# Kernel optimization log

Measured on AMD Instinct MI355X. Metric: run time of the kernel, lower is better.

## Reference

```python
import jax, jax.numpy as jnp
import numpy as np


def gatv2(x, src, dst, ea, Wl, bl, Wr, br, We, att, bias, N):
    # PyG GATv2Conv: source/target projections, edge embedding, leaky_relu(0.2)
    # attention, segment softmax over incoming edges, scatter-add aggregation.
    H, C = att.shape
    xl = (x @ Wl.T + bl).reshape(-1, H, C)   # [N,H,C] (source / message features)
    xr = (x @ Wr.T + br).reshape(-1, H, C)   # [N,H,C] (target features)
    ee = (ea @ We.T).reshape(-1, H, C)       # [E,H,C] edge embedding
    e = jax.nn.leaky_relu(xl[src] + xr[dst] + ee, 0.2)   # [E,H,C]
    s = jnp.einsum('ehc,hc->eh', e, att)                  # [E,H] scores
    smax = jax.ops.segment_max(s, dst, num_segments=N)
    ex = jnp.exp(s - smax[dst])
    den = jax.ops.segment_sum(ex, dst, num_segments=N)
    a = ex / (den[dst] + 1e-16)                           # segment softmax
    out = jax.ops.segment_sum(a[:, :, None] * xl[src], dst, num_segments=N)
    return out.reshape(N, H * C) + bias


def _forward(x, edge_index, edge_attr, actions, Wl1, bl1, Wr1, br1, We1, att1, bias1,
             Wl2, bl2, Wr2, br2, We2, att2, bias2, Wf, bf, Wp, bp, alpha):
    N = x.shape[0]
    E = edge_attr.shape[0]
    num_actions = E + 1
    src, dst = edge_index[0], edge_index[1]
    # add_self_loops(fill_value='mean'): self-loop edge_attr = per-node mean of incoming edge_attr
    cnt = jax.ops.segment_sum(jnp.ones((E,), x.dtype), dst, num_segments=N)
    mean_ea = jax.ops.segment_sum(edge_attr, dst, num_segments=N) / jnp.maximum(cnt, 1.0)[:, None]
    loop = jnp.arange(N, dtype=src.dtype)
    src2 = jnp.concatenate([src, loop])
    dst2 = jnp.concatenate([dst, loop])
    ea2 = jnp.concatenate([edge_attr, mean_ea], axis=0)
    h = jax.nn.relu(gatv2(x, src2, dst2, ea2, Wl1, bl1, Wr1, br1, We1, att1, bias1, N))
    h = jax.nn.relu(gatv2(h, src2, dst2, ea2, Wl2, bl2, Wr2, br2, We2, att2, bias2, N))
    g = jnp.mean(h, axis=0, keepdims=True)              # global_mean_pool, single graph -> [1,hid]
    state_potential = jax.nn.relu(g @ Wp.T + bp)[:, 0]  # [1]
    diag = jnp.concatenate([src != dst, jnp.array([True])])  # [E+1]
    logits = (g @ Wf.T + bf)[:, :num_actions]           # [1, E+1]
    amask = jnp.ones((num_actions,), bool).at[actions].set(False)
    mask = amask & diag
    logits = jnp.where(mask[None, :], logits, -jnp.inf)
    return jax.nn.softmax(logits, axis=1), state_potential, jax.nn.sigmoid(alpha)


def setup_inputs() -> dict:
    key = jax.random.key(0)
    ks = jax.random.split(key, 16)
    N, E, F, hid, H, A = 20000, 400000, 128, 64, 4, 450000
    x = jax.random.normal(ks[0], (N, F), jnp.float32)
    src = jax.random.randint(ks[1], (E,), 0, N)
    dst = (src + 1 + jax.random.randint(ks[2], (E,), 0, N - 1)) % N  # no pre-existing self loops
    edge_index = jnp.stack([src, dst])
    edge_attr = jax.random.normal(ks[3], (E, 1), jnp.float32)
    actions = jax.random.randint(ks[4], (128,), 0, E + 1)
    s = 0.05
    nrm = lambda k, shp: jax.random.normal(k, shp, jnp.float32) * s
    return {
        'x': x, 'edge_index': edge_index, 'edge_attr': edge_attr, 'actions': actions,
        'Wl1': nrm(ks[5], (H * hid, F)), 'bl1': jnp.zeros(H * hid),
        'Wr1': nrm(ks[6], (H * hid, F)), 'br1': jnp.zeros(H * hid),
        'We1': nrm(ks[7], (H * hid, 1)), 'att1': nrm(ks[8], (H, hid)), 'bias1': jnp.zeros(H * hid),
        'Wl2': nrm(ks[9], (hid, H * hid)), 'bl2': jnp.zeros(hid),
        'Wr2': nrm(ks[10], (hid, H * hid)), 'br2': jnp.zeros(hid),
        'We2': nrm(ks[11], (hid, 1)), 'att2': nrm(ks[12], (1, hid)), 'bias2': jnp.zeros(hid),
        'Wf': nrm(ks[13], (A, hid)), 'bf': jnp.zeros(A),
        'Wp': nrm(ks[14], (1, hid)), 'bp': jnp.zeros(1),
        'alpha': jnp.asarray(0.0, jnp.float32),
    }


def reference(x, edge_index, edge_attr, actions, Wl1, bl1, Wr1, br1, We1, att1, bias1,
              Wl2, bl2, Wr2, br2, We2, att2, bias2, Wf, bf, Wp, bp, alpha):
    return _forward(x, edge_index, edge_attr, actions, Wl1, bl1, Wr1, br1, We1, att1, bias1,
                    Wl2, bl2, Wr2, br2, We2, att2, bias2, Wf, bf, Wp, bp, alpha)
```

## Files before the change

### kernel.cpp

```cpp
#include <hip/hip_runtime.h>
#include <math.h>

typedef __attribute__((ext_vector_type(8))) short short8;
typedef __attribute__((ext_vector_type(4))) float f32x4;

__device__ __forceinline__ float wred_sum(float v) {
#pragma unroll
  for (int off = 32; off; off >>= 1) v += __shfl_xor(v, off, 64);
  return v;
}
__device__ __forceinline__ float wred_max(float v) {
#pragma unroll
  for (int off = 32; off; off >>= 1) v = fmaxf(v, __shfl_xor(v, off, 64));
  return v;
}
__device__ __forceinline__ unsigned f2key(float x) {
  unsigned b = __float_as_uint(x);
  return (b & 0x80000000u) ? ~b : (b | 0x80000000u);
}
__device__ __forceinline__ float key2f(unsigned k) {
  unsigned b = (k & 0x80000000u) ? (k & 0x7FFFFFFFu) : ~k;
  return __uint_as_float(b);
}
__device__ __forceinline__ float b2f(unsigned short u) {
  return __uint_as_float(((unsigned)u) << 16);
}
__device__ __forceinline__ unsigned short f2b(float f) {
  unsigned b = __float_as_uint(f);
  return (unsigned short)((b + 0x7FFFu + ((b >> 16) & 1u)) >> 16);
}

__global__ __launch_bounds__(256) void k_prep(
    const float* __restrict__ s0, ushort* __restrict__ d0, int n0,
    const float* __restrict__ s1, ushort* __restrict__ d1, int n1,
    const float* __restrict__ s2, ushort* __restrict__ d2, int n2,
    const float* __restrict__ s3, ushort* __restrict__ d3, int n3,
    const float* __restrict__ s4, ushort* __restrict__ d4, int n4,
    const float* __restrict__ Wf, ushort* __restrict__ wfT8, int NAp,
    const int* __restrict__ dstv, const float* __restrict__ ea,
    int* __restrict__ cnt_i, float* __restrict__ sum_ea, int E,
    int castB, int twfB) {
  __shared__ ushort lds[64][68];
  int b = blockIdx.x, tid = threadIdx.x;
  if (b < castB) {
    int t = (b * 256 + tid) * 4;
    const float* s; ushort* d; int off = t;
    if (off < n0) { s = s0; d = d0; }
    else { off -= n0;
      if (off < n1) { s = s1; d = d1; }
      else { off -= n1;
        if (off < n2) { s = s2; d = d2; }
        else { off -= n2;
          if (off < n3) { s = s3; d = d3; }
          else { off -= n3;
            if (off < n4) { s = s4; d = d4; }
            else return; } } } }
    float4 v = *(const float4*)(s + off);
    ushort4 o;
    o.x = f2b(v.x); o.y = f2b(v.y); o.z = f2b(v.z); o.w = f2b(v.w);
    *(ushort4*)(d + off) = o;
    return;
  }
  if (b < castB + twfB) {
    int row0 = (b - castB) * 64;
    int r = tid >> 2, cg = tid & 3;
    const float* srcp = Wf + ((size_t)(row0 + r)) * 64 + cg * 16;
#pragma unroll
    for (int u = 0; u < 4; ++u) {
      float4 v = *(const float4*)(srcp + u * 4);
      int c = cg * 16 + u * 4;
      lds[r][c + 0] = f2b(v.x); lds[r][c + 1] = f2b(v.y);
      lds[r][c + 2] = f2b(v.z); lds[r][c + 3] = f2b(v.w);
    }
    __syncthreads();
    int k8 = tid >> 5, rg = tid & 31;
#pragma unroll
    for (int h = 0; h < 2; ++h) {
      int r2 = rg + h * 32;
      ushort4 wa = *(const ushort4*)(&lds[r2][k8 * 8]);
      ushort4 wb = *(const ushort4*)(&lds[r2][k8 * 8 + 4]);
      ushort* dp = wfT8 + ((size_t)k8 * NAp + row0 + r2) * 8;
      *(ushort4*)(dp) = wa;
      *(ushort4*)(dp + 4) = wb;
    }
    return;
  }
  int e = (b - castB - twfB) * 256 + tid;
  if (e >= E) return;
  int d = dstv[e];
  atomicAdd(&cnt_i[d], 1);
  atomicAdd(&sum_ea[d], ea[e]);
}

__global__ __launch_bounds__(1024) void k_scan(const int* __restrict__ cnt_i,
    const float* __restrict__ sum_ea, float* __restrict__ mean_ea,
    int* __restrict__ row_st, int* __restrict__ cursor, int N) {
  __shared__ int ws[16];
  int tid = threadIdx.x;
  int lane = tid & 63, w = tid >> 6;
  int running = 0;
  for (int base = 0; base < N; base += 1024) {
    int i = base + tid;
    int c = 0;
    if (i < N) {
      int cc = cnt_i[i];
      c = cc + 1;
      mean_ea[i] = sum_ea[i] / fmaxf((float)cc, 1.0f);
    }
    int inc = c;
#pragma unroll
    for (int off = 1; off < 64; off <<= 1) {
      int u = __shfl_up(inc, off, 64);
      if (lane >= off) inc += u;
    }
    if (lane == 63) ws[w] = inc;
    __syncthreads();
    if (tid < 16) {
      int s = ws[tid];
#pragma unroll
      for (int off = 1; off < 16; off <<= 1) {
        int u = __shfl_up(s, off, 16);
        if (tid >= off) s += u;
      }
      ws[tid] = s;
    }
    __syncthreads();
    int woff = (w == 0) ? 0 : ws[w - 1];
    int total = ws[15];
    int ex = running + woff + (inc - c);
    if (i < N) { row_st[i] = ex; cursor[i] = ex; }
    running += total;
    __syncthreads();
  }
  if (tid == 0) row_st[N] = running;
}

__global__ __launch_bounds__(256) void k_gemm_scatter(const ushort* __restrict__ A,
    const ushort* __restrict__ W0, const float* __restrict__ b0, ushort* __restrict__ C0,
    const ushort* __restrict__ W1, const float* __restrict__ b1, ushort* __restrict__ C1,
    int M, int Nc, int K,
    const int* __restrict__ dstv, const int* __restrict__ srcv,
    const float* __restrict__ ea, const float* __restrict__ mean_ea,
    int* __restrict__ cursor, int* __restrict__ srcp, float* __restrict__ eap,
    int E, int E2) {
  int tid = threadIdx.x;
  if (blockIdx.z == 2) {
    int flat = blockIdx.x * gridDim.y + blockIdx.y;
    int stride = gridDim.x * gridDim.y * 256;
    for (int e = flat * 256 + tid; e < E2; e += stride) {
      int d, sn; float av;
      if (e < E) { d = dstv[e]; sn = srcv[e]; av = ea[e]; }
      else { d = e - E; sn = d; av = mean_ea[d]; }
      int pos = atomicAdd(&cursor[d], 1);
      srcp[pos] = sn;
      eap[pos] = av;
    }
    return;
  }
  const ushort* W = blockIdx.z ? W1 : W0;
  const float* bias = blockIdx.z ? b1 : b0;
  ushort* C = blockIdx.z ? C1 : C0;
  int wave = tid >> 6, lane = tid & 63;
  int m0 = blockIdx.x * 64 + wave * 16;
  int n0 = blockIdx.y * 64;
  int r = lane & 15, g = lane >> 4;
  f32x4 acc[4] = {};
  int am = min(m0 + r, M - 1);
  const ushort* Arow = A + (size_t)am * K + g * 8;
  const ushort* Wrow = W + (size_t)(n0 + r) * K + g * 8;
  for (int k0 = 0; k0 < K; k0 += 32) {
    short8 a = *(const short8*)(const void*)(Arow + k0);
#pragma unroll
    for (int c = 0; c < 4; ++c) {
      short8 b = *(const short8*)(const void*)(Wrow + (size_t)c * 16 * K + k0);
      acc[c] = __builtin_amdgcn_mfma_f32_16x16x32_bf16(a, b, acc[c], 0, 0, 0);
    }
  }
#pragma unroll
  for (int c = 0; c < 4; ++c) {
    int gn = n0 + c * 16 + r;
    float bv = bias[gn];
#pragma unroll
    for (int j = 0; j < 4; ++j) {
      int gm = m0 + g * 4 + j;
      if (gm < M) C[(size_t)gm * Nc + gn] = f2b(acc[c][j] + bv);
    }
  }
}

__global__ __launch_bounds__(256) void k_gemm_mfma2(const ushort* __restrict__ A,
    const ushort* __restrict__ W0, const float* __restrict__ b0, ushort* __restrict__ C0,
    const ushort* __restrict__ W1, const float* __restrict__ b1, ushort* __restrict__ C1,
    int M, int Nc, int K) {
  const ushort* W = blockIdx.z ? W1 : W0;
  const float* bias = blockIdx.z ? b1 : b0;
  ushort* C = blockIdx.z ? C1 : C0;
  int wave = threadIdx.x >> 6, lane = threadIdx.x & 63;
  int m0 = blockIdx.x * 64 + wave * 16;
  int n0 = blockIdx.y * 64;
  int r = lane & 15, g = lane >> 4;
  f32x4 acc[4] = {};
  int am = min(m0 + r, M - 1);
  const ushort* Arow = A + (size_t)am * K + g * 8;
  const ushort* Wrow = W + (size_t)(n0 + r) * K + g * 8;
  for (int k0 = 0; k0 < K; k0 += 32) {
    short8 a = *(const short8*)(const void*)(Arow + k0);
#pragma unroll
    for (int c = 0; c < 4; ++c) {
      short8 b = *(const short8*)(const void*)(Wrow + (size_t)c * 16 * K + k0);
      acc[c] = __builtin_amdgcn_mfma_f32_16x16x32_bf16(a, b, acc[c], 0, 0, 0);
    }
  }
#pragma unroll
  for (int c = 0; c < 4; ++c) {
    int gn = n0 + c * 16 + r;
    float bv = bias[gn];
#pragma unroll
    for (int j = 0; j < 4; ++j) {
      int gm = m0 + g * 4 + j;
      if (gm < M) C[(size_t)gm * Nc + gn] = f2b(acc[c][j] + bv);
    }
  }
}

__global__ __launch_bounds__(256) void k_fused1(const ushort* __restrict__ xl,
    const ushort* __restrict__ xr, const int* __restrict__ srcp,
    const float* __restrict__ eap, const int* __restrict__ row_st,
    const float* __restrict__ We, const float* __restrict__ att,
    const float* __restrict__ bias, ushort* __restrict__ out, int N) {
  int tid = threadIdx.x;
  int lane = tid & 63;
  int half = lane >> 5, l32 = lane & 31;
  int n = blockIdx.x * 8 + (tid >> 6) * 2 + half;
  if (n >= N) return;
  int c0 = l32 * 8;
  float4 Wa = *(const float4*)(We + c0), Wb = *(const float4*)(We + c0 + 4);
  float4 Aa = *(const float4*)(att + c0), Ab = *(const float4*)(att + c0 + 4);
  float Wev[8] = {Wa.x, Wa.y, Wa.z, Wa.w, Wb.x, Wb.y, Wb.z, Wb.w};
  float atv[8] = {Aa.x, Aa.y, Aa.z, Aa.w, Ab.x, Ab.y, Ab.z, Ab.w};
  short8 xru = *(const short8*)(const void*)(xr + (size_t)n * 256 + c0);
  float xrf[8];
#pragma unroll
  for (int j = 0; j < 8; ++j) xrf[j] = b2f((unsigned short)xru[j]);
  int a = row_st[n], b = row_st[n + 1];
  float m = -INFINITY, den = 0.f;
  float acc[8] = {};
  int sn_nx = srcp[a];
  float av_nx = eap[a];
  for (int i = a; i < b; ++i) {
    int sn = sn_nx;
    float av = av_nx;
    short8 xu = *(const short8*)(const void*)(xl + (size_t)sn * 256 + c0);
    if (i + 1 < b) { sn_nx = srcp[i + 1]; av_nx = eap[i + 1]; }
    float x[8];
    float t = 0.f;
#pragma unroll
    for (int j = 0; j < 8; ++j) {
      x[j] = b2f((unsigned short)xu[j]);
      float v = x[j] + xrf[j] + av * Wev[j];
      v = v > 0.f ? v : 0.2f * v;
      t += atv[j] * v;
    }
    t += __shfl_xor(t, 1, 8);
    t += __shfl_xor(t, 2, 8);
    t += __shfl_xor(t, 4, 8);
    if (t > m) {
      float sc = __expf(m - t);
      m = t; den *= sc;
#pragma unroll
      for (int j = 0; j < 8; ++j) acc[j] *= sc;
    }
    float ex = __expf(t - m);
    den += ex;
#pragma unroll
    for (int j = 0; j < 8; ++j) acc[j] += ex * x[j];
  }
  float inv = 1.f / (den + 1e-16f);
  float4 Ba = *(const float4*)(bias + c0), Bb = *(const float4*)(bias + c0 + 4);
  float bv[8] = {Ba.x, Ba.y, Ba.z, Ba.w, Bb.x, Bb.y, Bb.z, Bb.w};
  short8 o;
#pragma unroll
  for (int j = 0; j < 8; ++j) o[j] = (short)f2b(fmaxf(acc[j] * inv + bv[j], 0.f));
  *(short8*)(void*)(out + (size_t)n * 256 + c0) = o;
}

__global__ __launch_bounds__(256) void k_fused2(const ushort* __restrict__ xl,
    const ushort* __restrict__ xr, const int* __restrict__ srcp,
    const float* __restrict__ eap, const int* __restrict__ row_st,
    const float* __restrict__ We, const float* __restrict__ att,
    const float* __restrict__ bias, float* __restrict__ g_sum, int N) {
  __shared__ float gred[4][64];
  int tid = threadIdx.x;
  int lane = tid & 63, w = tid >> 6;
  int sub = lane >> 3, l8 = lane & 7;
  int n = blockIdx.x * 32 + w * 8 + sub;
  bool valid = n < N;
  int c0 = l8 * 8;
  float4 Wa = *(const float4*)(We + c0), Wb = *(const float4*)(We + c0 + 4);
  float4 Aa = *(const float4*)(att + c0), Ab = *(const float4*)(att + c0 + 4);
  float Wev[8] = {Wa.x, Wa.y, Wa.z, Wa.w, Wb.x, Wb.y, Wb.z, Wb.w};
  float atv[8] = {Aa.x, Aa.y, Aa.z, Aa.w, Ab.x, Ab.y, Ab.z, Ab.w};
  float xrf[8] = {};
  if (valid) {
    short8 xru = *(const short8*)(const void*)(xr + (size_t)n * 64 + c0);
#pragma unroll
    for (int j = 0; j < 8; ++j) xrf[j] = b2f((unsigned short)xru[j]);
  }
  int a = 0, b = 0;
  if (valid) { a = row_st[n]; b = row_st[n + 1]; }
  float m = -INFINITY, den = 0.f;
  float acc[8] = {};
  int sn_nx = valid ? srcp[a] : 0;
  float av_nx = valid ? eap[a] : 0.f;
  for (int i = a; i < b; ++i) {
    int sn = sn_nx;
    float av = av_nx;
    short8 xu = *(const short8*)(const void*)(xl + (size_t)sn * 64 + c0);
    if (i + 1 < b) { sn_nx = srcp[i + 1]; av_nx = eap[i + 1]; }
    float x[8];
    float t = 0.f;
#pragma unroll
    for (int j = 0; j < 8; ++j) {
      x[j] = b2f((unsigned short)xu[j]);
      float v = x[j] + xrf[j] + av * Wev[j];
      v = v > 0.f ? v : 0.2f * v;
      t += atv[j] * v;
    }
    t += __shfl_xor(t, 1, 8);
    t += __shfl_xor(t, 2, 8);
    t += __shfl_xor(t, 4, 8);
    if (t > m) {
      float sc = __expf(m - t);
      m = t; den *= sc;
#pragma unroll
      for (int j = 0; j < 8; ++j) acc[j] *= sc;
    }
    float ex = __expf(t - m);
    den += ex;
#pragma unroll
    for (int j = 0; j < 8; ++j) acc[j] += ex * x[j];
  }
  float inv = 1.f / (den + 1e-16f);
  float4 Ba = *(const float4*)(bias + c0), Bb = *(const float4*)(bias + c0 + 4);
  float bv[8] = {Ba.x, Ba.y, Ba.z, Ba.w, Bb.x, Bb.y, Bb.z, Bb.w};
  float vals[8];
#pragma unroll
  for (int j = 0; j < 8; ++j)
    vals[j] = valid ? fmaxf(acc[j] * inv + bv[j], 0.f) : 0.f;
#pragma unroll
  for (int j = 0; j < 8; ++j) {
    float v = vals[j];
    v += __shfl_xor(v, 8, 64);
    v += __shfl_xor(v, 16, 64);
    v += __shfl_xor(v, 32, 64);
    vals[j] = v;
  }
  if (lane < 8) {
#pragma unroll
    for (int j = 0; j < 8; ++j) gred[w][lane * 8 + j] = vals[j];
  }
  __syncthreads();
  if (tid < 64)
    atomicAdd(&g_sum[tid], gred[0][tid] + gred[1][tid] + gred[2][tid] + gred[3][tid]);
}

__global__ __launch_bounds__(256) void k_logits(const float* __restrict__ g_sum,
    const float* __restrict__ Wp, const float* __restrict__ bp,
    const float* __restrict__ alpha, const int* __restrict__ actions, int n_act,
    const ushort* __restrict__ wfT8, const float* __restrict__ bf,
    const unsigned char* __restrict__ aflag, const int* __restrict__ src,
    const int* __restrict__ dst, float* __restrict__ logits,
    unsigned* __restrict__ gmax_key, float* __restrict__ out,
    int E, int NA, int NAp, float invN) {
  __shared__ float gs[64];
  __shared__ float wmax[4];
  int tid = threadIdx.x;
  if (tid < 64) gs[tid] = g_sum[tid] * invN;
  __syncthreads();
  if (blockIdx.x == 0 && tid < 64) {
    float t = wred_sum(gs[tid] * Wp[tid]);
    if (tid == 0) {
      float sp = t + bp[0];
      out[NA] = sp > 0.f ? sp : 0.f;
      out[NA + 1] = 1.f / (1.f + __expf(-alpha[0]));
    }
  }
  int r = blockIdx.x * 256 + tid;
  float val = -INFINITY;
  if (r < NA) {
    float acc = 0.f;
#pragma unroll
    for (int k8 = 0; k8 < 8; ++k8) {
      short8 w = *(const short8*)(const void*)(wfT8 + ((size_t)k8 * NAp + r) * 8);
#pragma unroll
      for (int j = 0; j < 8; ++j)
        acc += b2f((unsigned short)w[j]) * gs[k8 * 8 + j];
    }
    bool keep = (!aflag[r]) && (r >= E || src[r] != dst[r]);
    val = keep ? (acc + bf[r]) : -INFINITY;
    logits[r] = val;
  }
  float mv = wred_max(val);
  if ((tid & 63) == 0) wmax[tid >> 6] = mv;
  __syncthreads();
  if (tid == 0) {
    float m = fmaxf(fmaxf(wmax[0], wmax[1]), fmaxf(wmax[2], wmax[3]));
    atomicMax(gmax_key, f2key(m));
  }
}

__global__ void k_aflag(const int* __restrict__ actions, unsigned char* __restrict__ aflag,
                        int n_act) {
  int i = threadIdx.x;
  if (i < n_act) aflag[actions[i]] = 1;
}

__global__ __launch_bounds__(256) void k_exp(float* __restrict__ logits,
    const unsigned* __restrict__ gmax_key, float* __restrict__ gsum, int NA) {
  __shared__ float wsum[4];
  int i = (blockIdx.x * 256 + threadIdx.x) * 4;
  float gmax = key2f(*gmax_key);
  float s = 0.f;
  if (i < NA) {
    float4 v = *(const float4*)(logits + i);
    float4 e;
    e.x = (i + 0 < NA && v.x != -INFINITY) ? __expf(v.x - gmax) : 0.f;
    e.y = (i + 1 < NA && v.y != -INFINITY) ? __expf(v.y - gmax) : 0.f;
    e.z = (i + 2 < NA && v.z != -INFINITY) ? __expf(v.z - gmax) : 0.f;
    e.w = (i + 3 < NA && v.w != -INFINITY) ? __expf(v.w - gmax) : 0.f;
    *(float4*)(logits + i) = e;
    s = e.x + e.y + e.z + e.w;
  }
  s = wred_sum(s);
  if ((threadIdx.x & 63) == 0) wsum[threadIdx.x >> 6] = s;
  __syncthreads();
  if (threadIdx.x == 0)
    atomicAdd(gsum, wsum[0] + wsum[1] + wsum[2] + wsum[3]);
}

__global__ __launch_bounds__(256) void k_norm(const float* __restrict__ logits,
    const float* __restrict__ gsum, float* __restrict__ out, int NA) {
  int i = (blockIdx.x * 256 + threadIdx.x) * 4;
  if (i >= NA) return;
  float inv = 1.f / (*gsum);
  if (i + 3 < NA) {
    float4 v = *(const float4*)(logits + i);
    float4 o;
    o.x = v.x * inv; o.y = v.y * inv; o.z = v.z * inv; o.w = v.w * inv;
    *(float4*)(out + i) = o;
  } else {
    for (int j = i; j < NA; ++j) out[j] = logits[j] * inv;
  }
}

extern "C" void kernel_launch(void* const* d_in, const int* in_sizes, int n_in,
                              void* d_out, int out_size, void* d_ws, size_t ws_size,
                              hipStream_t stream) {
  const float* x      = (const float*)d_in[0];
  const int*   eidx   = (const int*)d_in[1];
  const float* eattr  = (const float*)d_in[2];
  const int*   actions= (const int*)d_in[3];
  const float* Wl1 = (const float*)d_in[4];
  const float* bl1 = (const float*)d_in[5];
  const float* Wr1 = (const float*)d_in[6];
  const float* br1 = (const float*)d_in[7];
  const float* We1 = (const float*)d_in[8];
  const float* att1= (const float*)d_in[9];
  const float* bias1=(const float*)d_in[10];
  const float* Wl2 = (const float*)d_in[11];
  const float* bl2 = (const float*)d_in[12];
  const float* Wr2 = (const float*)d_in[13];
  const float* br2 = (const float*)d_in[14];
  const float* We2 = (const float*)d_in[15];
  const float* att2= (const float*)d_in[16];
  const float* bias2=(const float*)d_in[17];
  const float* Wf  = (const float*)d_in[18];
  const float* bf  = (const float*)d_in[19];
  const float* Wp  = (const float*)d_in[20];
  const float* bp  = (const float*)d_in[21];
  const float* alpha=(const float*)d_in[22];

  const int F = 128;
  const int N = in_sizes[0] / F;
  const int E = in_sizes[2];
  const int E2 = E + N;
  const int NA = E + 1;
  const int NAp = ((NA + 63) / 64) * 64;
  const int n_act = in_sizes[3];
  const int* src = eidx;
  const int* dst = eidx + E;

  float* ws = (float*)d_ws;
  size_t p = 0;
  int*      cnt_i    = (int*)(ws + p);      p += (size_t)N;
  float*    sum_ea   = ws + p;              p += (size_t)N;
  float*    g_sum    = ws + p;              p += 64;
  unsigned* gmax_key = (unsigned*)(ws + p); p += 64;
  float*    gsum     = ws + p;              p += 64;
  unsigned char* aflag = (unsigned char*)(ws + p); p += ((size_t)NA + 3) / 4;
  size_t zero_bytes = p * sizeof(float);
  float*    mean_ea  = ws + p;              p += (size_t)N;
  int*      row_st   = (int*)(ws + p);      p += (size_t)N + 64;
  int*      cursor   = (int*)(ws + p);      p += (size_t)N;
  int*      srcp     = (int*)(ws + p);      p += (size_t)E2;
  float*    eap      = ws + p;              p += (size_t)E2;
  float*    logits   = ws + p;              p += (size_t)NA + 64;
  p = (p + 3) & ~(size_t)3;
  ushort* ub = (ushort*)(ws + p);
  size_t q = 0;
  ushort* xb   = ub + q; q += (size_t)N * F;
  ushort* wl1b = ub + q; q += (size_t)256 * 128;
  ushort* wr1b = ub + q; q += (size_t)256 * 128;
  ushort* wl2b = ub + q; q += (size_t)64 * 256;
  ushort* wr2b = ub + q; q += (size_t)64 * 256;
  ushort* wfT8 = ub + q; q += (size_t)64 * NAp;
  ushort* xl1b = ub + q; q += (size_t)N * 256;
  ushort* xr1b = ub + q; q += (size_t)N * 256;
  ushort* h1b  = ub + q; q += (size_t)N * 256;
  ushort* xl2b = ub + q; q += (size_t)N * 64;
  ushort* xr2b = ub + q; q += (size_t)N * 64;

  float* out = (float*)d_out;

  hipMemsetAsync(d_ws, 0, zero_bytes, stream);

  {
    int n0 = N * F, n1 = 256 * 128, n2 = 256 * 128, n3 = 64 * 256, n4 = 64 * 256;
    int tot4 = (n0 + n1 + n2 + n3 + n4) / 4;
    int castB = (tot4 + 255) / 256;
    int twfB = NAp / 64;
    int cntB = (E + 255) / 256;
    k_prep<<<castB + twfB + cntB, 256, 0, stream>>>(
        x, xb, n0, Wl1, wl1b, n1, Wr1, wr1b, n2, Wl2, wl2b, n3, Wr2, wr2b, n4,
        Wf, wfT8, NAp, dst, eattr, cnt_i, sum_ea, E, castB, twfB);
  }

  k_scan<<<1, 1024, 0, stream>>>(cnt_i, sum_ea, mean_ea, row_st, cursor, N);

  {
    dim3 g1((N + 63) / 64, 4, 3);
    k_gemm_scatter<<<g1, 256, 0, stream>>>(xb, wl1b, bl1, xl1b, wr1b, br1, xr1b,
                                           N, 256, 128,
                                           dst, src, eattr, mean_ea, cursor,
                                           srcp, eap, E, E2);
  }
  k_fused1<<<(N + 7) / 8, 256, 0, stream>>>(xl1b, xr1b, srcp, eap, row_st,
                                            We1, att1, bias1, h1b, N);
  {
    dim3 g2((N + 63) / 64, 1, 2);
    k_gemm_mfma2<<<g2, 256, 0, stream>>>(h1b, wl2b, bl2, xl2b, wr2b, br2, xr2b,
                                         N, 64, 256);
  }
  k_fused2<<<(N + 31) / 32, 256, 0, stream>>>(xl2b, xr2b, srcp, eap, row_st,
                                              We2, att2, bias2, g_sum, N);

  k_aflag<<<1, 128, 0, stream>>>(actions, aflag, n_act);
  k_logits<<<(NA + 255) / 256, 256, 0, stream>>>(
      g_sum, Wp, bp, alpha, actions, n_act, wfT8, bf, aflag, src, dst,
      logits, gmax_key, out, E, NA, NAp, 1.0f / (float)N);
  int nb4 = (NA + 1023) / 1024;
  k_exp<<<nb4, 256, 0, stream>>>(logits, gmax_key, gsum, NA);
  k_norm<<<nb4, 256, 0, stream>>>(logits, gsum, out, NA);
}
```

Before: 279.0 us.

## Read fp32 Wf directly in logits kernel, drop bf16 transpose and aflag launch

Removes the bf16 transposed copy of Wf built in the prep kernel. The logits kernel now reads fp32 Wf rows directly, with four threads per row and a shuffle reduction. The action-flag marking moves into the prep kernel, which removes one launch. The global max is spread across 64 atomic slots and reduced in the exp kernel to cut atomic contention. The fp32 read doubles Wf bytes in the logits pass but avoids the separate cast and transpose pass plus its write and reread.

```diff
diff --git a/kernel.cpp b/kernel.cpp
--- a/kernel.cpp
+++ b/kernel.cpp
@@ -36,12 +36,12 @@
     const float* __restrict__ s2, ushort* __restrict__ d2, int n2,
     const float* __restrict__ s3, ushort* __restrict__ d3, int n3,
     const float* __restrict__ s4, ushort* __restrict__ d4, int n4,
-    const float* __restrict__ Wf, ushort* __restrict__ wfT8, int NAp,
     const int* __restrict__ dstv, const float* __restrict__ ea,
     int* __restrict__ cnt_i, float* __restrict__ sum_ea, int E,
-    int castB, int twfB) {
-  __shared__ ushort lds[64][68];
+    const int* __restrict__ actions, unsigned char* __restrict__ aflag,
+    int n_act, int castB) {
   int b = blockIdx.x, tid = threadIdx.x;
+  if (b == 0 && tid < n_act) aflag[actions[tid]] = 1;
   if (b < castB) {
     int t = (b * 256 + tid) * 4;
     const float* s; ushort* d; int off = t;
@@ -61,31 +61,7 @@
     *(ushort4*)(d + off) = o;
     return;
   }
-  if (b < castB + twfB) {
-    int row0 = (b - castB) * 64;
-    int r = tid >> 2, cg = tid & 3;
-    const float* srcp = Wf + ((size_t)(row0 + r)) * 64 + cg * 16;
-#pragma unroll
-    for (int u = 0; u < 4; ++u) {
-      float4 v = *(const float4*)(srcp + u * 4);
-      int c = cg * 16 + u * 4;
-      lds[r][c + 0] = f2b(v.x); lds[r][c + 1] = f2b(v.y);
-      lds[r][c + 2] = f2b(v.z); lds[r][c + 3] = f2b(v.w);
-    }
-    __syncthreads();
-    int k8 = tid >> 5, rg = tid & 31;
-#pragma unroll
-    for (int h = 0; h < 2; ++h) {
-      int r2 = rg + h * 32;
-      ushort4 wa = *(const ushort4*)(&lds[r2][k8 * 8]);
-      ushort4 wb = *(const ushort4*)(&lds[r2][k8 * 8 + 4]);
-      ushort* dp = wfT8 + ((size_t)k8 * NAp + row0 + r2) * 8;
-      *(ushort4*)(dp) = wa;
-      *(ushort4*)(dp + 4) = wb;
-    }
-    return;
-  }
-  int e = (b - castB - twfB) * 256 + tid;
+  int e = (b - castB) * 256 + tid;
   if (e >= E) return;
   int d = dstv[e];
   atomicAdd(&cnt_i[d], 1);
@@ -366,12 +342,12 @@
 
 __global__ __launch_bounds__(256) void k_logits(const float* __restrict__ g_sum,
     const float* __restrict__ Wp, const float* __restrict__ bp,
-    const float* __restrict__ alpha, const int* __restrict__ actions, int n_act,
-    const ushort* __restrict__ wfT8, const float* __restrict__ bf,
+    const float* __restrict__ alpha,
+    const float* __restrict__ Wf, const float* __restrict__ bf,
     const unsigned char* __restrict__ aflag, const int* __restrict__ src,
     const int* __restrict__ dst, float* __restrict__ logits,
     unsigned* __restrict__ gmax_key, float* __restrict__ out,
-    int E, int NA, int NAp, float invN) {
+    int E, int NA, float invN) {
   __shared__ float gs[64];
   __shared__ float wmax[4];
   int tid = threadIdx.x;
@@ -385,41 +361,43 @@
       out[NA + 1] = 1.f / (1.f + __expf(-alpha[0]));
     }
   }
-  int r = blockIdx.x * 256 + tid;
+  int j0 = tid & 3;
+  int row = blockIdx.x * 64 + (tid >> 2);
   float val = -INFINITY;
-  if (r < NA) {
+  if (row < NA) {
+    const float4* wr = (const float4*)(Wf + (size_t)row * 64);
+    const float4* g4 = (const float4*)gs;
     float acc = 0.f;
 #pragma unroll
-    for (int k8 = 0; k8 < 8; ++k8) {
-      short8 w = *(const short8*)(const void*)(wfT8 + ((size_t)k8 * NAp + r) * 8);
-#pragma unroll
-      for (int j = 0; j < 8; ++j)
-        acc += b2f((unsigned short)w[j]) * gs[k8 * 8 + j];
-    }
-    bool keep = (!aflag[r]) && (r >= E || src[r] != dst[r]);
-    val = keep ? (acc + bf[r]) : -INFINITY;
-    logits[r] = val;
+    for (int u = 0; u < 4; ++u) {
+      float4 w = wr[j0 + u * 4];
+      float4 gv = g4[j0 + u * 4];
+      acc += w.x * gv.x + w.y * gv.y + w.z * gv.z + w.w * gv.w;
+    }
+    acc += __shfl_xor(acc, 1, 4);
+    acc += __shfl_xor(acc, 2, 4);
+    if (j0 == 0) {
+      bool keep = (!aflag[row]) && (row >= E || src[row] != dst[row]);
+      val = keep ? (acc + bf[row]) : -INFINITY;
+      logits[row] = val;
+    }
   }
   float mv = wred_max(val);
   if ((tid & 63) == 0) wmax[tid >> 6] = mv;
   __syncthreads();
   if (tid == 0) {
     float m = fmaxf(fmaxf(wmax[0], wmax[1]), fmaxf(wmax[2], wmax[3]));
-    atomicMax(gmax_key, f2key(m));
-  }
-}
-
-__global__ void k_aflag(const int* __restrict__ actions, unsigned char* __restrict__ aflag,
-                        int n_act) {
-  int i = threadIdx.x;
-  if (i < n_act) aflag[actions[i]] = 1;
+    atomicMax(&gmax_key[blockIdx.x & 63], f2key(m));
+  }
 }
 
 __global__ __launch_bounds__(256) void k_exp(float* __restrict__ logits,
     const unsigned* __restrict__ gmax_key, float* __restrict__ gsum, int NA) {
   __shared__ float wsum[4];
-  int i = (blockIdx.x * 256 + threadIdx.x) * 4;
-  float gmax = key2f(*gmax_key);
+  int tid = threadIdx.x;
+  float gmax = key2f(gmax_key[tid & 63]);
+  gmax = wred_max(gmax);
+  int i = (blockIdx.x * 256 + tid) * 4;
   float s = 0.f;
   if (i < NA) {
     float4 v = *(const float4*)(logits + i);
@@ -432,9 +410,9 @@
     s = e.x + e.y + e.z + e.w;
   }
   s = wred_sum(s);
-  if ((threadIdx.x & 63) == 0) wsum[threadIdx.x >> 6] = s;
+  if ((tid & 63) == 0) wsum[tid >> 6] = s;
   __syncthreads();
-  if (threadIdx.x == 0)
+  if (tid == 0)
     atomicAdd(gsum, wsum[0] + wsum[1] + wsum[2] + wsum[3]);
 }
 
@@ -485,7 +463,6 @@
   const int E = in_sizes[2];
   const int E2 = E + N;
   const int NA = E + 1;
-  const int NAp = ((NA + 63) / 64) * 64;
   const int n_act = in_sizes[3];
   const int* src = eidx;
   const int* dst = eidx + E;
@@ -513,7 +490,6 @@
   ushort* wr1b = ub + q; q += (size_t)256 * 128;
   ushort* wl2b = ub + q; q += (size_t)64 * 256;
   ushort* wr2b = ub + q; q += (size_t)64 * 256;
-  ushort* wfT8 = ub + q; q += (size_t)64 * NAp;
   ushort* xl1b = ub + q; q += (size_t)N * 256;
   ushort* xr1b = ub + q; q += (size_t)N * 256;
   ushort* h1b  = ub + q; q += (size_t)N * 256;
@@ -528,11 +504,10 @@
     int n0 = N * F, n1 = 256 * 128, n2 = 256 * 128, n3 = 64 * 256, n4 = 64 * 256;
     int tot4 = (n0 + n1 + n2 + n3 + n4) / 4;
     int castB = (tot4 + 255) / 256;
-    int twfB = NAp / 64;
     int cntB = (E + 255) / 256;
-    k_prep<<<castB + twfB + cntB, 256, 0, stream>>>(
+    k_prep<<<castB + cntB, 256, 0, stream>>>(
         x, xb, n0, Wl1, wl1b, n1, Wr1, wr1b, n2, Wl2, wl2b, n3, Wr2, wr2b, n4,
-        Wf, wfT8, NAp, dst, eattr, cnt_i, sum_ea, E, castB, twfB);
+        dst, eattr, cnt_i, sum_ea, E, actions, aflag, n_act, castB);
   }
 
   k_scan<<<1, 1024, 0, stream>>>(cnt_i, sum_ea, mean_ea, row_st, cursor, N);
@@ -554,10 +529,9 @@
   k_fused2<<<(N + 31) / 32, 256, 0, stream>>>(xl2b, xr2b, srcp, eap, row_st,
                                               We2, att2, bias2, g_sum, N);
 
-  k_aflag<<<1, 128, 0, stream>>>(actions, aflag, n_act);
-  k_logits<<<(NA + 255) / 256, 256, 0, stream>>>(
-      g_sum, Wp, bp, alpha, actions, n_act, wfT8, bf, aflag, src, dst,
-      logits, gmax_key, out, E, NA, NAp, 1.0f / (float)N);
+  k_logits<<<(NA + 63) / 64, 256, 0, stream>>>(
+      g_sum, Wp, bp, alpha, Wf, bf, aflag, src, dst,
+      logits, gmax_key, out, E, NA, 1.0f / (float)N);
   int nb4 = (NA + 1023) / 1024;
   k_exp<<<nb4, 256, 0, stream>>>(logits, gmax_key, gsum, NA);
   k_norm<<<nb4, 256, 0, stream>>>(logits, gsum, out, NA);
```

Measured after the change: 272.0 us. -2.5%, faster.
